# Kernel tuning notes

Measured on AMD Instinct MI355X. Metric: run time of the kernel, lower is better.

The kernel has to match this reference:

```python
import jax, jax.numpy as jnp
import numpy as np

D = 512
HEADS = 4
DIM_HEAD = 128
SCALE = DIM_HEAD ** -0.5
A_NUMS = 60
N_NUMS = 60
DEPTH = 2


def _layer_norm(x, g, b, eps=1e-5):
    m = jnp.mean(x, axis=-1, keepdims=True)
    v = jnp.var(x, axis=-1, keepdims=True)
    return (x - m) * jax.lax.rsqrt(v + eps) * g + b


def _attention(x, qkv_w, out_w, out_b):
    B, T, _ = x.shape
    qkv = x @ qkv_w  # [B,T,3*H*Dh]
    q, k, v = jnp.split(qkv, 3, axis=-1)
    to_heads = lambda t: t.reshape(B, T, HEADS, DIM_HEAD).transpose(0, 2, 1, 3)
    q, k, v = to_heads(q), to_heads(k), to_heads(v)
    att = jax.nn.softmax(jnp.einsum('bhid,bhjd->bhij', q, k) * SCALE, axis=-1)
    o = jnp.einsum('bhij,bhjd->bhid', att, v).transpose(0, 2, 1, 3).reshape(B, T, HEADS * DIM_HEAD)
    return o @ out_w + out_b


def _memory(x, mem, nums):
    # sigmoid similarity to memory slots, topk-mean temporal score, weighted readout
    att = jax.nn.sigmoid(jnp.einsum('btd,kd->btk', x, mem) / jnp.sqrt(jnp.float32(D)))
    vals, _ = jax.lax.top_k(att, nums // 16 + 1)
    temporal_att = vals.mean(-1)  # [B,T]
    aug = jnp.einsum('btk,kd->btd', att, mem)
    return temporal_att, aug


def _topk_gather_mean(att, feats, k):
    _, idx = jax.lax.top_k(att, k)  # [B,k]
    g = jnp.take_along_axis(feats, idx[:, :, None], axis=1)  # [B,k,D]
    return g.mean(1), idx


def _l2norm(x):
    return x / jnp.linalg.norm(x, axis=-1, keepdims=True)


def setup_inputs():
    key = jax.random.key(0)
    ks = jax.random.split(key, 12)
    b, t, din = 64, 256, 1024
    s = 0.02
    return {
        'x': jax.random.normal(ks[0], (b, t, din), jnp.float32),
        'epsilon': jax.random.normal(ks[1], (b // 2, t, D), jnp.float32),
        'conv_w': jax.random.normal(ks[2], (D, din, 3), jnp.float32) * s,
        'conv_b': jnp.zeros((D,), jnp.float32),
        'ln1_g': jnp.ones((DEPTH, D), jnp.float32),
        'ln1_b': jnp.zeros((DEPTH, D), jnp.float32),
        'qkv_w': jax.random.normal(ks[3], (DEPTH, D, 3 * HEADS * DIM_HEAD), jnp.float32) * s,
        'out_w': jax.random.normal(ks[4], (DEPTH, HEADS * DIM_HEAD, D), jnp.float32) * s,
        'out_b': jnp.zeros((DEPTH, D), jnp.float32),
        'ln2_g': jnp.ones((DEPTH, D), jnp.float32),
        'ln2_b': jnp.zeros((DEPTH, D), jnp.float32),
        'ff1_w': jax.random.normal(ks[5], (DEPTH, D, D), jnp.float32) * s,
        'ff1_b': jnp.zeros((DEPTH, D), jnp.float32),
        'ff2_w': jax.random.normal(ks[6], (DEPTH, D, D), jnp.float32) * s,
        'ff2_b': jnp.zeros((DEPTH, D), jnp.float32),
        'a_mem': jax.random.normal(ks[7], (A_NUMS, D), jnp.float32) * s,
        'n_mem': jax.random.normal(ks[8], (N_NUMS, D), jnp.float32) * s,
        'mu_w': jax.random.normal(ks[9], (D, D), jnp.float32) * s,
        'mu_b': jnp.zeros((D,), jnp.float32),
        'var_w': jax.random.normal(ks[10], (D, D), jnp.float32) * s,
        'var_b': jnp.zeros((D,), jnp.float32),
    }


def reference(x, epsilon, conv_w, conv_b, ln1_g, ln1_b, qkv_w, out_w, out_b,
              ln2_g, ln2_b, ff1_w, ff1_b, ff2_w, ff2_b, a_mem, n_mem,
              mu_w, mu_b, var_w, var_b):
    b, t, _ = x.shape
    # Temporal embedding: Conv1d(k=3, pad=1) + ReLU
    h = jax.lax.conv_general_dilated(x.transpose(0, 2, 1), conv_w, (1,), [(1, 1)],
                                     dimension_numbers=('NCH', 'OIH', 'NCH'))
    h = jax.nn.relu(h + conv_b[None, :, None]).transpose(0, 2, 1)  # [B,T,512]
    # Transformer: PreNorm attn + PreNorm FF, residual, depth=2
    for i in range(DEPTH):
        h = h + _attention(_layer_norm(h, ln1_g[i], ln1_b[i]), qkv_w[i], out_w[i], out_b[i])
        f = _layer_norm(h, ln2_g[i], ln2_b[i])
        f = jax.nn.gelu(f @ ff1_w[i] + ff1_b[i], approximate=False)
        h = h + f @ ff2_w[i] + ff2_b[i]
    x_emb = h
    v_feat = x_emb.transpose(0, 2, 1)
    half = b // 2
    N_x, A_x = x_emb[:half], x_emb[half:]
    A_att, A_aug = _memory(A_x, a_mem, A_NUMS)
    N_Aatt, N_Aaug = _memory(A_x, n_mem, N_NUMS)
    A_Natt, A_Naug = _memory(N_x, a_mem, A_NUMS)
    N_att, N_aug = _memory(N_x, n_mem, N_NUMS)
    k = t // 16 + 1
    negative_ax, A_idx = _topk_gather_mean(A_att, A_x, k)
    anchor_nx, N_idx = _topk_gather_mean(N_att, N_x, k)
    positive_nx, _ = _topk_gather_mean(N_Aatt, A_x, k)
    eps = 1e-6
    an, ap, ng = _l2norm(anchor_nx), _l2norm(positive_nx), _l2norm(negative_ax)
    dp = jnp.linalg.norm(an - ap + eps, axis=-1)
    dn = jnp.linalg.norm(an - ng + eps, axis=-1)
    triplet = jnp.mean(jax.nn.relu(dp - dn + 1.0))
    N_aug_mu = N_aug @ mu_w + mu_b
    N_aug_var = N_aug @ var_w + var_b
    N_aug_new = N_aug_mu + epsilon * jnp.sqrt(jnp.exp(N_aug_var))
    anchor_nx_new = jnp.take_along_axis(N_aug_new, N_idx[:, :, None], axis=1).mean(1)
    A_aug_new = A_aug @ mu_w + mu_b
    negative_ax_new = jnp.take_along_axis(A_aug_new, A_idx[:, :, None], axis=1).mean(1)
    kl_loss = jnp.mean(-0.5 * jnp.sum(1.0 + N_aug_var - N_aug_mu ** 2 - jnp.exp(N_aug_var), axis=1))
    A_Naug_m = A_Naug @ mu_w + mu_b
    N_Aaug_m = N_Aaug @ mu_w + mu_b
    na = jnp.maximum(jnp.linalg.norm(anchor_nx, axis=1), eps)
    nn_ = jnp.maximum(jnp.linalg.norm(negative_ax, axis=1), eps)
    cos_loss = jnp.mean(1.0 - jnp.sum(anchor_nx * negative_ax, axis=1) / (na * nn_))
    distance = jnp.mean(jax.nn.relu(100.0 - jnp.linalg.norm(negative_ax_new, axis=-1)
                                    + jnp.linalg.norm(anchor_nx_new, axis=-1)))
    aug_cat = jnp.concatenate([N_aug_new + A_Naug_m, A_aug_new + N_Aaug_m], axis=0)
    x_out = jnp.concatenate([x_emb, aug_cat], axis=-1)  # [B,T,1024]
    return (triplet, kl_loss, distance, A_att, N_att, A_Natt, N_Aatt, cos_loss, x_out, v_feat)
```

## Files before the change

### kernel.cpp

```cpp
#include <hip/hip_runtime.h>
#include <math.h>

namespace {

typedef unsigned short u16;
typedef __attribute__((ext_vector_type(8))) short s8v;
typedef __attribute__((ext_vector_type(8))) unsigned short u16x8;
typedef __attribute__((ext_vector_type(4))) float f32x4;
typedef __attribute__((ext_vector_type(4))) unsigned int u32x4;

constexpr int HBT = 8192;
constexpr long HHf = 4194304;

constexpr long F_H    = 0;
constexpr long F_LNB  = 8388608;
constexpr long F_QKV  = 12582912;
constexpr long F_VT   = 25165824;
constexpr long F_SC   = 29360128;
constexpr long F_ATT  = 12582912;
constexpr long F_AUG  = 14548992;
constexpr long F_MU   = 22937600;
constexpr long F_VAR  = 27131904;
constexpr long F_R0   = 31326208;
constexpr long F_R1   = 35520512;
constexpr long F_R2   = 39714816;
constexpr long W_MEMB = 43909120;
constexpr long Z_PG   = 43939840;
constexpr long W_QKV  = 46137344;
constexpr long W_OUT  = 46923776;
constexpr long W_FF1  = 47185920;
constexpr long W_FF2  = 47448064;
constexpr long W_MU   = 47710208;
constexpr long W_VAR  = 47841280;
constexpr long W_CONV = 47972352;
constexpr long W_AMT  = 48758784;
constexpr long W_NMT  = 48775168;
constexpr long O_ANC  = 48791552;
constexpr long O_POS  = O_ANC + 16384;
constexpr long O_NEG  = O_POS + 16384;
constexpr long O_ANEW = O_NEG + 16384;
constexpr long O_NNEG = O_ANEW + 16384;
constexpr long O_IDX  = O_NNEG + 16384;
constexpr long O_ACC  = O_IDX + 1632;

constexpr long OO_AATT  = 3;
constexpr long OO_NATT  = 3 + 8192;
constexpr long OO_ANATT = 3 + 16384;
constexpr long OO_NAATT = 3 + 24576;
constexpr long OO_COS   = 32771;
constexpr long OO_XOUT  = 32772;
constexpr long OO_VFEAT = 32772L + 16777216L;

__device__ inline u16 to_bf16(float f) {
  union { float f; unsigned u; } x; x.f = f;
  unsigned r = x.u + 0x7fffu + ((x.u >> 16) & 1u);
  return (u16)(r >> 16);
}
__device__ inline u16x8 pack8(float4 a, float4 b) {
  u16x8 r;
  r[0]=to_bf16(a.x); r[1]=to_bf16(a.y); r[2]=to_bf16(a.z); r[3]=to_bf16(a.w);
  r[4]=to_bf16(b.x); r[5]=to_bf16(b.y); r[6]=to_bf16(b.z); r[7]=to_bf16(b.w);
  return r;
}

typedef __attribute__((address_space(1))) void gvoid;
typedef __attribute__((address_space(3))) void lvoid;
__device__ inline void gld16(const u16* g, u16* l) {
  __builtin_amdgcn_global_load_lds((gvoid*)g, (lvoid*)l, 16, 0, 0);
}

__device__ inline float bred_sum(float v, float* sm, int tid) {
  sm[tid] = v; __syncthreads();
  for (int s = 128; s > 0; s >>= 1) { if (tid < s) sm[tid] += sm[tid + s]; __syncthreads(); }
  float r = sm[0]; __syncthreads();
  return r;
}

struct GP2 {
  const void* A; const void* B; const float* bias; void* C;
  const float* bias2;
  int M, N, K, lda, ldb, ldc, Hdiv;
  long sAb, sAh, sBb, sBh, sCb, sCh;
  float scale;
};


template<int EPI, bool ABF, bool BBF, bool ACC, bool CBF, bool GL>
__global__ __launch_bounds__(256) void mgemm_k(GP2 p) {
  __shared__ __align__(16) u16 As[4096];
  __shared__ __align__(16) u16 Bs[4096];
  int bb = blockIdx.z / p.Hdiv, hh = blockIdx.z % p.Hdiv;
  long aoff = (long)bb * p.sAb + (long)hh * p.sAh;
  long boff = (long)bb * p.sBb + (long)hh * p.sBh;
  long coff = (long)bb * p.sCb + (long)hh * p.sCh;
  int m0 = blockIdx.x * 128, n0 = blockIdx.y * 128;
  int tid = threadIdx.x, r = tid & 127, seg = tid >> 7;
  int lane = tid & 63, wave = tid >> 6;
  int wm = (wave >> 1) * 64, wn = (wave & 1) * 64;
  int l15 = lane & 15, quad = lane >> 4;
  int rs = (r >> 1) & 3;
  int qs = (quad ^ ((l15 >> 1) & 3)) * 8;
  f32x4 acc[4][4] = {};
  for (int k0 = 0; k0 < p.K; k0 += 32) {
    if constexpr (GL) {
      int lr = lane >> 2;
      int lc = (((lane & 3) ^ ((lane >> 3) & 3)) * 8);
      const u16* Ab = (const u16*)p.A + aoff + (long)(m0 + wave * 16 + lr) * p.lda + k0 + lc;
      gld16(Ab,                    &As[wave * 512]);
      gld16(Ab + (long)64 * p.lda, &As[2048 + wave * 512]);
      const u16* Bb = (const u16*)p.B + boff + (long)(n0 + wave * 16 + lr) * p.ldb + k0 + lc;
      gld16(Bb,                    &Bs[wave * 512]);
      gld16(Bb + (long)64 * p.ldb, &Bs[2048 + wave * 512]);
    } else {
      bool kfull = (k0 + 32 <= p.K);
      int p0 = ((2 * seg) ^ rs) * 8;
      int p1 = ((2 * seg + 1) ^ rs) * 8;
      {
        int gm = m0 + r;
        if (ABF) {
          const u16* Ar = (const u16*)p.A + aoff + (long)gm * p.lda + k0 + seg * 16;
          if (kfull) {
            *(u32x4*)&As[r * 32 + p0] = *(const u32x4*)Ar;
            *(u32x4*)&As[r * 32 + p1] = *(const u32x4*)(Ar + 8);
          } else {
            for (int c = 0; c < 16; c++) {
              int kk = k0 + seg * 16 + c;
              int cc = seg * 16 + c;
              As[r * 32 + (((cc >> 3) ^ rs) << 3) + (cc & 7)] = (kk < p.K) ? Ar[c] : (u16)0;
            }
          }
        } else {
          const float* Ar = (const float*)p.A + aoff + (long)gm * p.lda + k0 + seg * 16;
          if (kfull) {
            float4 f0 = ((const float4*)Ar)[0];
            float4 f1 = ((const float4*)Ar)[1];
            float4 f2 = ((const float4*)Ar)[2];
            float4 f3 = ((const float4*)Ar)[3];
            *(u16x8*)&As[r * 32 + p0] = pack8(f0, f1);
            *(u16x8*)&As[r * 32 + p1] = pack8(f2, f3);
          } else {
            for (int c = 0; c < 16; c++) {
              int kk = k0 + seg * 16 + c;
              int cc = seg * 16 + c;
              As[r * 32 + (((cc >> 3) ^ rs) << 3) + (cc & 7)] = (kk < p.K) ? to_bf16(Ar[c]) : (u16)0;
            }
          }
        }
      }
      {
        int gn = n0 + r;
        bool nv = gn < p.N;
        if (BBF) {
          const u16* Br = (const u16*)p.B + boff + (long)gn * p.ldb + k0 + seg * 16;
          if (nv && kfull) {
            *(u32x4*)&Bs[r * 32 + p0] = *(const u32x4*)Br;
            *(u32x4*)&Bs[r * 32 + p1] = *(const u32x4*)(Br + 8);
          } else {
            for (int c = 0; c < 16; c++) {
              int kk = k0 + seg * 16 + c;
              int cc = seg * 16 + c;
              Bs[r * 32 + (((cc >> 3) ^ rs) << 3) + (cc & 7)] = (nv && kk < p.K) ? Br[c] : (u16)0;
            }
          }
        } else {
          const float* Br = (const float*)p.B + boff + (long)gn * p.ldb + k0 + seg * 16;
          if (nv && kfull) {
            float4 f0 = ((const float4*)Br)[0];
            float4 f1 = ((const float4*)Br)[1];
            float4 f2 = ((const float4*)Br)[2];
            float4 f3 = ((const float4*)Br)[3];
            *(u16x8*)&Bs[r * 32 + p0] = pack8(f0, f1);
            *(u16x8*)&Bs[r * 32 + p1] = pack8(f2, f3);
          } else {
            for (int c = 0; c < 16; c++) {
              int kk = k0 + seg * 16 + c;
              int cc = seg * 16 + c;
              Bs[r * 32 + (((cc >> 3) ^ rs) << 3) + (cc & 7)] = (nv && kk < p.K) ? to_bf16(Br[c]) : (u16)0;
            }
          }
        }
      }
    }
    __syncthreads();
    s8v af[4], bfr[4];
#pragma unroll
    for (int i = 0; i < 4; i++) af[i]  = *(const s8v*)&As[(wm + i * 16 + l15) * 32 + qs];
#pragma unroll
    for (int j = 0; j < 4; j++) bfr[j] = *(const s8v*)&Bs[(wn + j * 16 + l15) * 32 + qs];
#pragma unroll
    for (int i = 0; i < 4; i++)
#pragma unroll
      for (int j = 0; j < 4; j++)
        acc[i][j] = __builtin_amdgcn_mfma_f32_16x16x32_bf16(af[i], bfr[j], acc[i][j], 0, 0, 0);
    __syncthreads();
  }
  const float* bp = (p.bias2 && (hh & 1)) ? p.bias2 : p.bias;
#pragma unroll
  for (int j = 0; j < 4; j++) {
    int col = n0 + wn + j * 16 + l15;
    if (col >= p.N) continue;
    float bv = bp ? bp[col] : 0.f;
#pragma unroll
    for (int i = 0; i < 4; i++) {
#pragma unroll
      for (int rr = 0; rr < 4; rr++) {
        int row = m0 + wm + i * 16 + quad * 4 + rr;
        float v = acc[i][j][rr] * p.scale + bv;
        if (EPI == 1) v = 0.5f * v * (1.f + erff(v * 0.70710678118654752f));
        if (EPI == 2) v = 1.f / (1.f + expf(-v));
        long ci = coff + (long)row * p.ldc + col;
        if (CBF) ((u16*)p.C)[ci] = to_bf16(v);
        else {
          float* Cp = (float*)p.C;
          if (ACC) v += Cp[ci];
          Cp[ci] = v;
        }
      }
    }
  }
}

__global__ __launch_bounds__(256) void convm_k(const u16* __restrict__ xb,
    const u16* __restrict__ zp, const u16* __restrict__ wT,
    const float* __restrict__ bias, float* __restrict__ out) {
  __shared__ __align__(16) u16 As[4096];
  __shared__ __align__(16) u16 Bs[4096];
  int m0 = blockIdx.x * 128, n0 = blockIdx.y * 128;
  int b = m0 >> 8, tb = m0 & 255;
  int tid = threadIdx.x;
  int lane = tid & 63, wave = tid >> 6;
  int wm = (wave >> 1) * 64, wn = (wave & 1) * 64;
  int l15 = lane & 15, quad = lane >> 4;
  int lr = lane >> 2;
  int lc = (((lane & 3) ^ ((lane >> 3) & 3)) * 8);
  int qs = (quad ^ ((l15 >> 1) & 3)) * 8;
  int arow = wave * 16 + lr;
  f32x4 acc[4][4] = {};
  for (int k0 = 0; k0 < 3072; k0 += 32) {
    int kp = k0 >> 10, i0 = (k0 & 1023);
    int t2a = tb + arow + kp - 1;
    const u16* Aa = (t2a >= 0 && t2a < 256)
        ? xb + ((long)(b * 256 + t2a)) * 1024 + i0 + lc
        : zp + lc;
    gld16(Aa, &As[wave * 512]);
    int t2b = t2a + 64;
    const u16* Ab2 = (t2b >= 0 && t2b < 256)
        ? xb + ((long)(b * 256 + t2b)) * 1024 + i0 + lc
        : zp + lc;
    gld16(Ab2, &As[2048 + wave * 512]);
    const u16* Bb = wT + (long)(n0 + arow) * 3072 + k0 + lc;
    gld16(Bb,                   &Bs[wave * 512]);
    gld16(Bb + (long)64 * 3072, &Bs[2048 + wave * 512]);
    __syncthreads();
    s8v af[4], bfr[4];
#pragma unroll
    for (int i = 0; i < 4; i++) af[i]  = *(const s8v*)&As[(wm + i * 16 + l15) * 32 + qs];
#pragma unroll
    for (int j = 0; j < 4; j++) bfr[j] = *(const s8v*)&Bs[(wn + j * 16 + l15) * 32 + qs];
#pragma unroll
    for (int i = 0; i < 4; i++)
#pragma unroll
      for (int j = 0; j < 4; j++)
        acc[i][j] = __builtin_amdgcn_mfma_f32_16x16x32_bf16(af[i], bfr[j], acc[i][j], 0, 0, 0);
    __syncthreads();
  }
#pragma unroll
  for (int j = 0; j < 4; j++) {
    int col = n0 + wn + j * 16 + l15;
    float bv = bias[col];
#pragma unroll
    for (int i = 0; i < 4; i++)
#pragma unroll
      for (int rr = 0; rr < 4; rr++) {
        int row = m0 + wm + i * 16 + quad * 4 + rr;
        float v = acc[i][j][rr] + bv;
        out[(long)row * 512 + col] = v > 0.f ? v : 0.f;
      }
  }
}

__global__ __launch_bounds__(256) void wtrans_k(const float* __restrict__ src,
    u16* __restrict__ dst, int R, int C) {
  __shared__ float t[32][33];
  int c0 = blockIdx.x * 32, r0 = blockIdx.y * 32;
  int tx = threadIdx.x & 31, ty = threadIdx.x >> 5;
  for (int rr = 0; rr < 32; rr += 8)
    t[ty + rr][tx] = src[(long)(r0 + ty + rr) * C + c0 + tx];
  __syncthreads();
  for (int rr = 0; rr < 32; rr += 8)
    dst[(long)(c0 + ty + rr) * R + r0 + tx] = to_bf16(t[tx][ty + rr]);
}

__global__ __launch_bounds__(256) void convw_t(const float* __restrict__ src, u16* __restrict__ dst) {
  int id = blockIdx.x * 256 + threadIdx.x;
  if (id >= 512 * 3072) return;
  int o = id / 3072, r2 = id % 3072;
  int kp = r2 >> 10, i = r2 & 1023;
  dst[id] = to_bf16(src[(long)o * 3072 + i * 3 + kp]);
}

__global__ __launch_bounds__(256) void memtrans_k(const float* __restrict__ src, u16* __restrict__ dst) {
  int id = blockIdx.x * 256 + threadIdx.x;
  if (id >= 512 * 64) return;
  int n = id >> 6, k = id & 63;
  dst[id] = (k < 60) ? to_bf16(src[(long)k * 512 + n]) : (u16)0;
}

__global__ __launch_bounds__(256) void vtrans_k(const u16* __restrict__ qkv, u16* __restrict__ vt) {
  __shared__ u16 t[32][33];
  int z = blockIdx.z;
  int b = z >> 2, h2 = z & 3;
  int t0 = blockIdx.x * 32, d0 = blockIdx.y * 32;
  int tx = threadIdx.x & 31, ty = threadIdx.x >> 5;
  const u16* src = qkv + (long)b * 393216 + 1024 + h2 * 128;
  for (int rr = 0; rr < 32; rr += 8)
    t[ty + rr][tx] = src[(long)(t0 + ty + rr) * 1536 + d0 + tx];
  __syncthreads();
  u16* dst = vt + (long)z * 32768;
  for (int rr = 0; rr < 32; rr += 8)
    dst[(long)(d0 + ty + rr) * 256 + t0 + tx] = t[tx][ty + rr];
}

__global__ __launch_bounds__(256) void cvt_k(const float* __restrict__ src, u16* __restrict__ dst, long n) {
  long i = ((long)blockIdx.x * 256 + threadIdx.x) * 8;
  if (i >= n) return;
  float4 f0 = ((const float4*)(src + i))[0];
  float4 f1 = ((const float4*)(src + i))[1];
  *(u16x8*)(dst + i) = pack8(f0, f1);
}

__global__ void zpage_k(u16* __restrict__ z) { z[threadIdx.x] = 0; }

__global__ __launch_bounds__(256) void ln_k(const float* __restrict__ in,
    const float* __restrict__ g, const float* __restrict__ b, u16* __restrict__ out) {
  int wave = threadIdx.x >> 6, lane = threadIdx.x & 63;
  long row = (long)blockIdx.x * 4 + wave;
  const float* r = in + row * 512 + lane * 8;
  float4 x0 = ((const float4*)r)[0];
  float4 x1 = ((const float4*)r)[1];
  float s = x0.x + x0.y + x0.z + x0.w + x1.x + x1.y + x1.z + x1.w;
  for (int off = 32; off; off >>= 1) s += __shfl_xor(s, off);
  float mean = s * (1.f / 512.f);
  float d[8] = {x0.x - mean, x0.y - mean, x0.z - mean, x0.w - mean,
                x1.x - mean, x1.y - mean, x1.z - mean, x1.w - mean};
  float q = 0.f;
#pragma unroll
  for (int i = 0; i < 8; i++) q += d[i] * d[i];
  for (int off = 32; off; off >>= 1) q += __shfl_xor(q, off);
  float inv = rsqrtf(q * (1.f / 512.f) + 1e-5f);
  const float4* gp = (const float4*)(g + lane * 8);
  const float4* bp = (const float4*)(b + lane * 8);
  float4 g0 = gp[0], g1 = gp[1], b0 = bp[0], b1 = bp[1];
  float gv[8] = {g0.x, g0.y, g0.z, g0.w, g1.x, g1.y, g1.z, g1.w};
  float bv[8] = {b0.x, b0.y, b0.z, b0.w, b1.x, b1.y, b1.z, b1.w};
  u16x8 o;
#pragma unroll
  for (int i = 0; i < 8; i++) o[i] = to_bf16(d[i] * inv * gv[i] + bv[i]);
  *(u16x8*)(out + row * 512 + lane * 8) = o;
}

__global__ __launch_bounds__(256) void softmax_k(float* __restrict__ s) {
  int wave = threadIdx.x >> 6, lane = threadIdx.x & 63;
  long row = (long)blockIdx.x * 4 + wave;
  float* r = s + row * 256 + lane * 4;
  float4 v = *(float4*)r;
  float mx = fmaxf(fmaxf(v.x, v.y), fmaxf(v.z, v.w));
  for (int off = 32; off; off >>= 1) mx = fmaxf(mx, __shfl_xor(mx, off));
  v.x = expf(v.x - mx); v.y = expf(v.y - mx); v.z = expf(v.z - mx); v.w = expf(v.w - mx);
  float sum = v.x + v.y + v.z + v.w;
  for (int off = 32; off; off >>= 1) sum += __shfl_xor(sum, off);
  float is = 1.f / sum;
  v.x *= is; v.y *= is; v.z *= is; v.w *= is;
  *(float4*)r = v;
}

__global__ __launch_bounds__(256) void top4_k(const float* __restrict__ att, float* __restrict__ out) {
  int y = blockIdx.y;
  int i = blockIdx.x * 256 + threadIdx.x;
  if (i >= HBT) return;
  const float* a = att + (long)y * 491520 + (long)i * 60;
  float t0 = -1e30f, t1 = -1e30f, t2 = -1e30f, t3 = -1e30f;
  for (int k = 0; k < 60; k++) {
    float v = a[k];
    if (v > t0)      { t3 = t2; t2 = t1; t1 = t0; t0 = v; }
    else if (v > t1) { t3 = t2; t2 = t1; t1 = v; }
    else if (v > t2) { t3 = t2; t2 = v; }
    else if (v > t3) { t3 = v; }
  }
  int ooff = (y == 0) ? 0 : (4 - y) * 8192;
  out[ooff + i] = (t0 + t1 + t2 + t3) * 0.25f;
}

__global__ __launch_bounds__(256) void topk17_k(const float* __restrict__ tatt, int* __restrict__ idx) {
  int b = blockIdx.x, y = blockIdx.y, tid = threadIdx.x;
  __shared__ float sv[256];
  __shared__ int si[256];
  float v = tatt[(long)y * 8192 + (long)b * 256 + tid];
  int* ob = idx + y * 544 + b * 17;
  for (int s = 0; s < 17; s++) {
    sv[tid] = v; si[tid] = tid;
    __syncthreads();
    for (int off = 128; off > 0; off >>= 1) {
      if (tid < off) {
        float v2 = sv[tid + off]; int i2 = si[tid + off];
        if (v2 > sv[tid] || (v2 == sv[tid] && i2 < si[tid])) { sv[tid] = v2; si[tid] = i2; }
      }
      __syncthreads();
    }
    int win = si[0];
    if (tid == 0) ob[s] = win;
    if (tid == win) v = -1e30f;
    __syncthreads();
  }
}

__device__ inline void gmean_body(const float* feats, const int* idx, float* out, int b, int tid) {
  float s0 = 0.f, s1 = 0.f;
  for (int j = 0; j < 17; j++) {
    int t = idx[b * 17 + j];
    const float* r = feats + ((long)b * 256 + t) * 512;
    s0 += r[tid]; s1 += r[tid + 256];
  }
  out[(long)b * 512 + tid]       = s0 * (1.f / 17.f);
  out[(long)b * 512 + tid + 256] = s1 * (1.f / 17.f);
}

__global__ __launch_bounds__(256) void gmean3_k(const float* __restrict__ Ax,
    const float* __restrict__ Nx, const int* __restrict__ idx0, float* __restrict__ ob) {
  int b = blockIdx.x, y = blockIdx.y, tid = threadIdx.x;
  const float* feats = (y == 1) ? Nx : Ax;
  const int* idx = idx0 + y * 544;
  float* out = ob + (long)((y + 2) % 3) * 16384;
  gmean_body(feats, idx, out, b, tid);
}

__global__ __launch_bounds__(256) void gmean2_k(const float* __restrict__ f0,
    const float* __restrict__ f1, const int* __restrict__ idx0, float* __restrict__ ob) {
  int b = blockIdx.x, y = blockIdx.y, tid = threadIdx.x;
  const float* feats = y ? f1 : f0;
  const int* idx = idx0 + (y == 0 ? 544 : 0);
  float* out = ob + (long)y * 16384;
  gmean_body(feats, idx, out, b, tid);
}

__global__ __launch_bounds__(256) void vae_k(const float* __restrict__ mu,
    const float* __restrict__ var, const float* __restrict__ eps,
    float* __restrict__ nnew, float* __restrict__ accum) {
  constexpr long N4 = HHf / 4;
  long stride = (long)gridDim.x * 256;
  float kle = 0.f;
  for (long i = (long)blockIdx.x * 256 + threadIdx.x; i < N4; i += stride) {
    float4 m4 = ((const float4*)mu)[i];
    float4 v4 = ((const float4*)var)[i];
    float4 e4 = ((const float4*)eps)[i];
    float4 o;
    float ev;
    ev = expf(v4.x); o.x = m4.x + e4.x * sqrtf(ev); kle += 1.f + v4.x - m4.x * m4.x - ev;
    ev = expf(v4.y); o.y = m4.y + e4.y * sqrtf(ev); kle += 1.f + v4.y - m4.y * m4.y - ev;
    ev = expf(v4.z); o.z = m4.z + e4.z * sqrtf(ev); kle += 1.f + v4.z - m4.z * m4.z - ev;
    ev = expf(v4.w); o.w = m4.w + e4.w * sqrtf(ev); kle += 1.f + v4.w - m4.w * m4.w - ev;
    ((float4*)nnew)[i] = o;
  }
  __shared__ float sm[256];
  float s = bred_sum(kle, sm, threadIdx.x);
  if (threadIdx.x == 0) atomicAdd(accum + 0, s);
}

__global__ __launch_bounds__(256) void tripcos_k(const float* __restrict__ anc,
    const float* __restrict__ pos, const float* __restrict__ neg, float* __restrict__ accum) {
  int b = blockIdx.x, tid = threadIdx.x;
  const float *a = anc + (long)b * 512, *p = pos + (long)b * 512, *n = neg + (long)b * 512;
  float a0 = a[tid], a1 = a[tid + 256], p0 = p[tid], p1 = p[tid + 256], n0 = n[tid], n1 = n[tid + 256];
  __shared__ float sm[256];
  float sa  = bred_sum(a0 * a0 + a1 * a1, sm, tid);
  float sp  = bred_sum(p0 * p0 + p1 * p1, sm, tid);
  float sn  = bred_sum(n0 * n0 + n1 * n1, sm, tid);
  float dot = bred_sum(a0 * n0 + a1 * n1, sm, tid);
  float na = sqrtf(sa), np_ = sqrtf(sp), nn = sqrtf(sn);
  float ina = 1.f / na, inp = 1.f / np_, inn = 1.f / nn;
  float d0 = a0 * ina - p0 * inp + 1e-6f, d1 = a1 * ina - p1 * inp + 1e-6f;
  float e0 = a0 * ina - n0 * inn + 1e-6f, e1 = a1 * ina - n1 * inn + 1e-6f;
  float dp2 = bred_sum(d0 * d0 + d1 * d1, sm, tid);
  float dn2 = bred_sum(e0 * e0 + e1 * e1, sm, tid);
  if (tid == 0) {
    float dp = sqrtf(dp2), dn = sqrtf(dn2);
    float t = dp - dn + 1.f;
    atomicAdd(accum + 1, t > 0.f ? t : 0.f);
    float c = 1.f - dot / (fmaxf(na, 1e-6f) * fmaxf(nn, 1e-6f));
    atomicAdd(accum + 2, c);
  }
}

__global__ __launch_bounds__(256) void dist_k(const float* __restrict__ anew,
    const float* __restrict__ nneg, float* __restrict__ accum) {
  int b = blockIdx.x, tid = threadIdx.x;
  const float *a = anew + (long)b * 512, *n = nneg + (long)b * 512;
  float a0 = a[tid], a1 = a[tid + 256], n0 = n[tid], n1 = n[tid + 256];
  __shared__ float sm[256];
  float sa = bred_sum(a0 * a0 + a1 * a1, sm, tid);
  float sn = bred_sum(n0 * n0 + n1 * n1, sm, tid);
  if (tid == 0) {
    float v = 100.f - sqrtf(sn) + sqrtf(sa);
    atomicAdd(accum + 3, v > 0.f ? v : 0.f);
  }
}

__global__ __launch_bounds__(256) void xout_k(const float* __restrict__ emb,
    const float* __restrict__ nnew, const float* __restrict__ anm,
    const float* __restrict__ anew, const float* __restrict__ nam,
    float* __restrict__ xout) {
  long i = (long)blockIdx.x * 256 + threadIdx.x;
  long row = i >> 9;
  int d = (int)(i & 511);
  long o = row * 1024 + d;
  xout[o] = emb[i];
  float v;
  if (i < HHf) v = nnew[i] + anm[i];
  else         v = anew[i - HHf] + nam[i - HHf];
  xout[o + 512] = v;
}

__global__ __launch_bounds__(256) void vfeat_k(const float* __restrict__ emb, float* __restrict__ vf) {
  __shared__ float tile[32][33];
  int b = blockIdx.z;
  int t0 = blockIdx.x * 32, d0 = blockIdx.y * 32;
  int tx = threadIdx.x & 31, ty = threadIdx.x >> 5;
  for (int r = 0; r < 32; r += 8)
    tile[ty + r][tx] = emb[((long)b * 256 + t0 + ty + r) * 512 + d0 + tx];
  __syncthreads();
  for (int r = 0; r < 32; r += 8)
    vf[((long)b * 512 + d0 + ty + r) * 256 + t0 + tx] = tile[tx][ty + r];
}

__global__ void init_k(float* accum) {
  accum[0] = 0.f; accum[1] = 0.f; accum[2] = 0.f; accum[3] = 0.f;
}

__global__ void fin_k(const float* __restrict__ accum, float* __restrict__ out) {
  out[0] = accum[1] * (1.f / 32.f);
  out[1] = -0.5f * accum[0] * (1.f / 16384.f);
  out[2] = accum[3] * (1.f / 32.f);
  out[OO_COS] = accum[2] * (1.f / 32.f);
}

static inline GP2 mk(const void* A, const void* B, const float* bias, void* C,
                     int M, int N, int K, int lda, int ldb, int ldc,
                     float scale = 1.f, int Hdiv = 1,
                     long sAb = 0, long sAh = 0, long sBb = 0, long sBh = 0,
                     long sCb = 0, long sCh = 0, const float* bias2 = nullptr) {
  GP2 p; p.A = A; p.B = B; p.bias = bias; p.C = C; p.bias2 = bias2;
  p.M = M; p.N = N; p.K = K; p.lda = lda; p.ldb = ldb; p.ldc = ldc;
  p.Hdiv = Hdiv; p.sAb = sAb; p.sAh = sAh; p.sBb = sBb; p.sBh = sBh;
  p.sCb = sCb; p.sCh = sCh; p.scale = scale;
  return p;
}

}

extern "C" void kernel_launch(void* const* d_in, const int* in_sizes, int n_in,
                              void* d_out, int out_size, void* d_ws, size_t ws_size,
                              hipStream_t stream) {
  const float* x      = (const float*)d_in[0];
  const float* epsi   = (const float*)d_in[1];
  const float* conv_w = (const float*)d_in[2];
  const float* conv_b = (const float*)d_in[3];
  const float* ln1_g  = (const float*)d_in[4];
  const float* ln1_b  = (const float*)d_in[5];
  const float* qkv_w  = (const float*)d_in[6];
  const float* out_w  = (const float*)d_in[7];
  const float* out_b  = (const float*)d_in[8];
  const float* ln2_g  = (const float*)d_in[9];
  const float* ln2_b  = (const float*)d_in[10];
  const float* ff1_w  = (const float*)d_in[11];
  const float* ff1_b  = (const float*)d_in[12];
  const float* ff2_w  = (const float*)d_in[13];
  const float* ff2_b  = (const float*)d_in[14];
  const float* a_mem  = (const float*)d_in[15];
  const float* n_mem  = (const float*)d_in[16];
  const float* mu_w   = (const float*)d_in[17];
  const float* mu_b   = (const float*)d_in[18];
  const float* var_w  = (const float*)d_in[19];
  const float* var_b  = (const float*)d_in[20];
  float* out = (float*)d_out;
  float* ws  = (float*)d_ws;

  const float ATTSCALE = 0.08838834764831845f;
  const float SIGSCALE = 0.04419417382415922f;

  float* h   = ws + F_H;
  u16* lnb   = (u16*)(ws + F_LNB);
  u16* qkvb  = (u16*)(ws + F_QKV);
  u16* vtb   = (u16*)(ws + F_VT);
  float* scf = ws + F_SC;
  u16* wqkvT = (u16*)(ws + W_QKV);
  u16* woutT = (u16*)(ws + W_OUT);
  u16* wff1T = (u16*)(ws + W_FF1);
  u16* wff2T = (u16*)(ws + W_FF2);
  u16* wmuT  = (u16*)(ws + W_MU);
  u16* wvarT = (u16*)(ws + W_VAR);
  u16* wconvT= (u16*)(ws + W_CONV);
  u16* amtT  = (u16*)(ws + W_AMT);
  u16* nmtT  = (u16*)(ws + W_NMT);
  u16* membT = (u16*)(ws + W_MEMB);
  u16* zpage = (u16*)(ws + Z_PG);
  u16* xb    = (u16*)(ws + F_QKV);

  wtrans_k<<<dim3(48, 16), 256, 0, stream>>>(qkv_w,          wqkvT,          512, 1536);
  wtrans_k<<<dim3(48, 16), 256, 0, stream>>>(qkv_w + 786432, wqkvT + 786432, 512, 1536);
  wtrans_k<<<dim3(16, 16), 256, 0, stream>>>(out_w,          woutT,          512, 512);
  wtrans_k<<<dim3(16, 16), 256, 0, stream>>>(out_w + 262144, woutT + 262144, 512, 512);
  wtrans_k<<<dim3(16, 16), 256, 0, stream>>>(ff1_w,          wff1T,          512, 512);
  wtrans_k<<<dim3(16, 16), 256, 0, stream>>>(ff1_w + 262144, wff1T + 262144, 512, 512);
  wtrans_k<<<dim3(16, 16), 256, 0, stream>>>(ff2_w,          wff2T,          512, 512);
  wtrans_k<<<dim3(16, 16), 256, 0, stream>>>(ff2_w + 262144, wff2T + 262144, 512, 512);
  wtrans_k<<<dim3(16, 16), 256, 0, stream>>>(mu_w,           wmuT,           512, 512);
  wtrans_k<<<dim3(16, 16), 256, 0, stream>>>(var_w,          wvarT,          512, 512);
  convw_t<<<6144, 256, 0, stream>>>(conv_w, wconvT);
  memtrans_k<<<128, 256, 0, stream>>>(a_mem, amtT);
  memtrans_k<<<128, 256, 0, stream>>>(n_mem, nmtT);

  cvt_k<<<8192, 256, 0, stream>>>(x, xb, 16777216);
  zpage_k<<<1, 256, 0, stream>>>(zpage);
  convm_k<<<dim3(128, 4), 256, 0, stream>>>(xb, zpage, wconvT, conv_b, h);

  for (int i = 0; i < 2; i++) {
    ln_k<<<4096, 256, 0, stream>>>(h, ln1_g + i * 512, ln1_b + i * 512, lnb);
    {
      GP2 p = mk(lnb, wqkvT + (long)i * 786432, nullptr, qkvb, 16384, 1536, 512, 512, 512, 1536);
      mgemm_k<0, true, true, false, true, true><<<dim3(128, 12, 1), 256, 0, stream>>>(p);
    }
    vtrans_k<<<dim3(8, 4, 256), 256, 0, stream>>>(qkvb, vtb);
    {
      GP2 p = mk(qkvb, qkvb + 512, nullptr, scf, 256, 256, 128, 1536, 1536, 256,
                 ATTSCALE, 4, 393216, 128, 393216, 128, 262144, 65536);
      mgemm_k<0, true, true, false, false, true><<<dim3(2, 2, 256), 256, 0, stream>>>(p);
    }
    softmax_k<<<16384, 256, 0, stream>>>(scf);
    {
      GP2 p = mk(scf, vtb, nullptr, lnb, 256, 128, 256, 256, 256, 512,
                 1.f, 4, 262144, 65536, 131072, 32768, 131072, 128);
      mgemm_k<0, false, true, false, true, false><<<dim3(2, 1, 256), 256, 0, stream>>>(p);
    }
    {
      GP2 p = mk(lnb, woutT + (long)i * 262144, out_b + i * 512, h, 16384, 512, 512, 512, 512, 512);
      mgemm_k<0, true, true, true, false, true><<<dim3(128, 4, 1), 256, 0, stream>>>(p);
    }
    ln_k<<<4096, 256, 0, stream>>>(h, ln2_g + i * 512, ln2_b + i * 512, lnb);
    {
      GP2 p = mk(lnb, wff1T + (long)i * 262144, ff1_b + i * 512, qkvb, 16384, 512, 512, 512, 512, 512);
      mgemm_k<1, true, true, false, true, true><<<dim3(128, 4, 1), 256, 0, stream>>>(p);
    }
    {
      GP2 p = mk(qkvb, wff2T + (long)i * 262144, ff2_b + i * 512, h, 16384, 512, 512, 512, 512, 512);
      mgemm_k<0, true, true, true, false, true><<<dim3(128, 4, 1), 256, 0, stream>>>(p);
    }
  }

  u16* hb = lnb;
  cvt_k<<<4096, 256, 0, stream>>>(h, hb, 8388608);
  cvt_k<<<15, 256, 0, stream>>>(a_mem, membT, 30720);
  cvt_k<<<15, 256, 0, stream>>>(n_mem, membT + 30720, 30720);
  const float* Nx = h;
  const float* Ax = h + HHf;
  const u16* Axb = hb + HHf;
  float* attA  = ws + F_ATT;
  float* attN  = ws + F_ATT + 1474560;

  {
    GP2 p = mk(Axb, membT, nullptr, attA, HBT, 60, 512, 512, 512, 60, SIGSCALE,
               2, -(long)HHf, 0, 0, 30720, 983040, 491520);
    mgemm_k<2, true, true, false, false, false><<<dim3(64, 1, 4), 256, 0, stream>>>(p);
  }

  top4_k<<<dim3(32, 4), 256, 0, stream>>>(attA, out + OO_AATT);

  u16* augb = (u16*)(ws + F_AUG);
  u16* augA  = augb;
  u16* augN  = augb + 3 * HHf;
  {
    GP2 p = mk(attA, amtT, nullptr, augA, HBT, 512, 60, 60, 64, 512, 1.f,
               2, 983040, 491520, 0, 32768, 2 * HHf, HHf);
    mgemm_k<0, false, true, false, true, false><<<dim3(64, 4, 4), 256, 0, stream>>>(p);
  }

  float* accum = ws + O_ACC;
  int* idxA = (int*)(ws + O_IDX);
  init_k<<<1, 1, 0, stream>>>(accum);

  topk17_k<<<dim3(32, 3), 256, 0, stream>>>(out + OO_AATT, idxA);
  gmean3_k<<<dim3(32, 3), 256, 0, stream>>>(Ax, Nx, idxA, ws + O_ANC);
  tripcos_k<<<32, 256, 0, stream>>>(ws + O_ANC, ws + O_POS, ws + O_NEG, accum);

  {
    GP2 p = mk(augN, wmuT, mu_b, ws + F_MU, HBT, 512, 512, 512, 512, 512, 1.f,
               2, 0, 0, 0, 262144, 0, 4194304, var_b);
    mgemm_k<0, true, true, false, false, true><<<dim3(64, 4, 2), 256, 0, stream>>>(p);
  }
  vae_k<<<512, 256, 0, stream>>>(ws + F_MU, ws + F_VAR, epsi, ws + F_MU, accum);

  {
    GP2 p = mk(augA, wmuT, mu_b, ws + F_R0, HBT, 512, 512, 512, 512, 512, 1.f,
               1, HHf, 0, 0, 0, 4194304, 0);
    mgemm_k<0, true, true, false, false, true><<<dim3(64, 4, 3), 256, 0, stream>>>(p);
  }

  gmean2_k<<<dim3(32, 2), 256, 0, stream>>>(ws + F_MU, ws + F_R0, idxA, ws + O_ANEW);
  dist_k<<<32, 256, 0, stream>>>(ws + O_ANEW, ws + O_NNEG, accum);

  xout_k<<<32768, 256, 0, stream>>>(h, ws + F_MU, ws + F_R2, ws + F_R0, ws + F_R1,
                                    out + OO_XOUT);
  vfeat_k<<<dim3(8, 16, 64), 256, 0, stream>>>(h, out + OO_VFEAT);
  fin_k<<<1, 1, 0, stream>>>(accum, out);
}
```

Before: 1.104 ms.

## Emit bf16 softmax probabilities, batch weight transposes, pad memory matrices

Softmax now writes bf16 probabilities into a separate buffer, so the attention-times-V GEMM reads half the bytes and can take its bf16/aligned fast path instead of converting fp32 on load. The eight 512x512 weight transposes are merged into one launch indexed by blockIdx.z, and the two memory transposes into one. The memory bank is zero-padded to 128 rows so the sigmoid-similarity GEMM can use its aligned path. The cost is bf16 rounding of the attention probabilities, plus a moved zero page to make room for the padded buffer.

Measured after the change: 962.0 us. 1.15x faster.

```diff
diff --git a/kernel.cpp b/kernel.cpp
--- a/kernel.cpp
+++ b/kernel.cpp
@@ -6,6 +6,7 @@
 typedef unsigned short u16;
 typedef __attribute__((ext_vector_type(8))) short s8v;
 typedef __attribute__((ext_vector_type(8))) unsigned short u16x8;
+typedef __attribute__((ext_vector_type(4))) unsigned short u16x4;
 typedef __attribute__((ext_vector_type(4))) float f32x4;
 typedef __attribute__((ext_vector_type(4))) unsigned int u32x4;
 
@@ -25,7 +26,7 @@
 constexpr long F_R1   = 35520512;
 constexpr long F_R2   = 39714816;
 constexpr long W_MEMB = 43909120;
-constexpr long Z_PG   = 43939840;
+constexpr long Z_PG   = 43974656;
 constexpr long W_QKV  = 46137344;
 constexpr long W_OUT  = 46923776;
 constexpr long W_FF1  = 47185920;
@@ -291,6 +292,21 @@
     dst[(long)(c0 + ty + rr) * R + r0 + tx] = to_bf16(t[tx][ty + rr]);
 }
 
+struct WT8 { const float* s[8]; long doff[8]; };
+__global__ __launch_bounds__(256) void wt8_k(WT8 w, u16* __restrict__ base) {
+  __shared__ float t[32][33];
+  int z = blockIdx.z;
+  const float* src = w.s[z];
+  u16* dst = base + w.doff[z];
+  int c0 = blockIdx.x * 32, r0 = blockIdx.y * 32;
+  int tx = threadIdx.x & 31, ty = threadIdx.x >> 5;
+  for (int rr = 0; rr < 32; rr += 8)
+    t[ty + rr][tx] = src[(long)(r0 + ty + rr) * 512 + c0 + tx];
+  __syncthreads();
+  for (int rr = 0; rr < 32; rr += 8)
+    dst[(long)(c0 + ty + rr) * 512 + r0 + tx] = to_bf16(t[tx][ty + rr]);
+}
+
 __global__ __launch_bounds__(256) void convw_t(const float* __restrict__ src, u16* __restrict__ dst) {
   int id = blockIdx.x * 256 + threadIdx.x;
   if (id >= 512 * 3072) return;
@@ -299,11 +315,23 @@
   dst[id] = to_bf16(src[(long)o * 3072 + i * 3 + kp]);
 }
 
-__global__ __launch_bounds__(256) void memtrans_k(const float* __restrict__ src, u16* __restrict__ dst) {
+__global__ __launch_bounds__(256) void memtrans2_k(const float* __restrict__ a,
+    const float* __restrict__ n, u16* __restrict__ amt, u16* __restrict__ nmt) {
   int id = blockIdx.x * 256 + threadIdx.x;
   if (id >= 512 * 64) return;
-  int n = id >> 6, k = id & 63;
-  dst[id] = (k < 60) ? to_bf16(src[(long)k * 512 + n]) : (u16)0;
+  const float* src = blockIdx.y ? n : a;
+  u16* dst = blockIdx.y ? nmt : amt;
+  int nn = id >> 6, k = id & 63;
+  dst[id] = (k < 60) ? to_bf16(src[(long)k * 512 + nn]) : (u16)0;
+}
+
+__global__ __launch_bounds__(256) void membpad_k(const float* __restrict__ a,
+    const float* __restrict__ n, u16* __restrict__ dst) {
+  int id = blockIdx.x * 256 + threadIdx.x;
+  int mat = id >> 16, r2 = id & 65535;
+  int nr = r2 >> 9, k = r2 & 511;
+  const float* s = mat ? n : a;
+  dst[id] = (nr < 60) ? to_bf16(s[(long)nr * 512 + k]) : (u16)0;
 }
 
 __global__ __launch_bounds__(256) void vtrans_k(const u16* __restrict__ qkv, u16* __restrict__ vt) {
@@ -359,19 +387,21 @@
   *(u16x8*)(out + row * 512 + lane * 8) = o;
 }
 
-__global__ __launch_bounds__(256) void softmax_k(float* __restrict__ s) {
+__global__ __launch_bounds__(256) void softmax_k(const float* __restrict__ s, u16* __restrict__ d) {
   int wave = threadIdx.x >> 6, lane = threadIdx.x & 63;
   long row = (long)blockIdx.x * 4 + wave;
-  float* r = s + row * 256 + lane * 4;
-  float4 v = *(float4*)r;
+  const float* r = s + row * 256 + lane * 4;
+  float4 v = *(const float4*)r;
   float mx = fmaxf(fmaxf(v.x, v.y), fmaxf(v.z, v.w));
   for (int off = 32; off; off >>= 1) mx = fmaxf(mx, __shfl_xor(mx, off));
   v.x = expf(v.x - mx); v.y = expf(v.y - mx); v.z = expf(v.z - mx); v.w = expf(v.w - mx);
   float sum = v.x + v.y + v.z + v.w;
   for (int off = 32; off; off >>= 1) sum += __shfl_xor(sum, off);
   float is = 1.f / sum;
-  v.x *= is; v.y *= is; v.z *= is; v.w *= is;
-  *(float4*)r = v;
+  u16x4 o;
+  o[0] = to_bf16(v.x * is); o[1] = to_bf16(v.y * is);
+  o[2] = to_bf16(v.z * is); o[3] = to_bf16(v.w * is);
+  *(u16x4*)(d + row * 256 + lane * 4) = o;
 }
 
 __global__ __launch_bounds__(256) void top4_k(const float* __restrict__ att, float* __restrict__ out) {
@@ -592,12 +622,12 @@
   u16* qkvb  = (u16*)(ws + F_QKV);
   u16* vtb   = (u16*)(ws + F_VT);
   float* scf = ws + F_SC;
+  u16* scb   = qkvb;
   u16* wqkvT = (u16*)(ws + W_QKV);
   u16* woutT = (u16*)(ws + W_OUT);
   u16* wff1T = (u16*)(ws + W_FF1);
   u16* wff2T = (u16*)(ws + W_FF2);
   u16* wmuT  = (u16*)(ws + W_MU);
-  u16* wvarT = (u16*)(ws + W_VAR);
   u16* wconvT= (u16*)(ws + W_CONV);
   u16* amtT  = (u16*)(ws + W_AMT);
   u16* nmtT  = (u16*)(ws + W_NMT);
@@ -607,17 +637,20 @@
 
   wtrans_k<<<dim3(48, 16), 256, 0, stream>>>(qkv_w,          wqkvT,          512, 1536);
   wtrans_k<<<dim3(48, 16), 256, 0, stream>>>(qkv_w + 786432, wqkvT + 786432, 512, 1536);
-  wtrans_k<<<dim3(16, 16), 256, 0, stream>>>(out_w,          woutT,          512, 512);
-  wtrans_k<<<dim3(16, 16), 256, 0, stream>>>(out_w + 262144, woutT + 262144, 512, 512);
-  wtrans_k<<<dim3(16, 16), 256, 0, stream>>>(ff1_w,          wff1T,          512, 512);
-  wtrans_k<<<dim3(16, 16), 256, 0, stream>>>(ff1_w + 262144, wff1T + 262144, 512, 512);
-  wtrans_k<<<dim3(16, 16), 256, 0, stream>>>(ff2_w,          wff2T,          512, 512);
-  wtrans_k<<<dim3(16, 16), 256, 0, stream>>>(ff2_w + 262144, wff2T + 262144, 512, 512);
-  wtrans_k<<<dim3(16, 16), 256, 0, stream>>>(mu_w,           wmuT,           512, 512);
-  wtrans_k<<<dim3(16, 16), 256, 0, stream>>>(var_w,          wvarT,          512, 512);
+  {
+    WT8 w;
+    w.s[0] = out_w;          w.doff[0] = 2 * W_OUT;
+    w.s[1] = out_w + 262144; w.doff[1] = 2 * W_OUT + 262144;
+    w.s[2] = ff1_w;          w.doff[2] = 2 * W_FF1;
+    w.s[3] = ff1_w + 262144; w.doff[3] = 2 * W_FF1 + 262144;
+    w.s[4] = ff2_w;          w.doff[4] = 2 * W_FF2;
+    w.s[5] = ff2_w + 262144; w.doff[5] = 2 * W_FF2 + 262144;
+    w.s[6] = mu_w;           w.doff[6] = 2 * W_MU;
+    w.s[7] = var_w;          w.doff[7] = 2 * W_VAR;
+    wt8_k<<<dim3(16, 16, 8), 256, 0, stream>>>(w, (u16*)ws);
+  }
   convw_t<<<6144, 256, 0, stream>>>(conv_w, wconvT);
-  memtrans_k<<<128, 256, 0, stream>>>(a_mem, amtT);
-  memtrans_k<<<128, 256, 0, stream>>>(n_mem, nmtT);
+  memtrans2_k<<<dim3(128, 2), 256, 0, stream>>>(a_mem, n_mem, amtT, nmtT);
 
   cvt_k<<<8192, 256, 0, stream>>>(x, xb, 16777216);
   zpage_k<<<1, 256, 0, stream>>>(zpage);
@@ -635,11 +668,11 @@
                  ATTSCALE, 4, 393216, 128, 393216, 128, 262144, 65536);
       mgemm_k<0, true, true, false, false, true><<<dim3(2, 2, 256), 256, 0, stream>>>(p);
     }
-    softmax_k<<<16384, 256, 0, stream>>>(scf);
+    softmax_k<<<16384, 256, 0, stream>>>(scf, scb);
     {
-      GP2 p = mk(scf, vtb, nullptr, lnb, 256, 128, 256, 256, 256, 512,
+      GP2 p = mk(scb, vtb, nullptr, lnb, 256, 128, 256, 256, 256, 512,
                  1.f, 4, 262144, 65536, 131072, 32768, 131072, 128);
-      mgemm_k<0, false, true, false, true, false><<<dim3(2, 1, 256), 256, 0, stream>>>(p);
+      mgemm_k<0, true, true, false, true, true><<<dim3(2, 1, 256), 256, 0, stream>>>(p);
     }
     {
       GP2 p = mk(lnb, woutT + (long)i * 262144, out_b + i * 512, h, 16384, 512, 512, 512, 512, 512);
@@ -658,8 +691,7 @@
 
   u16* hb = lnb;
   cvt_k<<<4096, 256, 0, stream>>>(h, hb, 8388608);
-  cvt_k<<<15, 256, 0, stream>>>(a_mem, membT, 30720);
-  cvt_k<<<15, 256, 0, stream>>>(n_mem, membT + 30720, 30720);
+  membpad_k<<<512, 256, 0, stream>>>(a_mem, n_mem, membT);
   const float* Nx = h;
   const float* Ax = h + HHf;
   const u16* Axb = hb + HHf;
@@ -668,8 +700,8 @@
 
   {
     GP2 p = mk(Axb, membT, nullptr, attA, HBT, 60, 512, 512, 512, 60, SIGSCALE,
-               2, -(long)HHf, 0, 0, 30720, 983040, 491520);
-    mgemm_k<2, true, true, false, false, false><<<dim3(64, 1, 4), 256, 0, stream>>>(p);
+               2, -(long)HHf, 0, 0, 65536, 983040, 491520);
+    mgemm_k<2, true, true, false, false, true><<<dim3(64, 1, 4), 256, 0, stream>>>(p);
   }
 
   top4_k<<<dim3(32, 4), 256, 0, stream>>>(attA, out + OO_AATT);
```
